# Kernel tuning notes

Hardware: AMD Instinct MI355X
Metric: run time of the kernel (lower is better)

## Reference

```python
import jax, jax.numpy as jnp
import numpy as np

H = 16      # num_heads
DK = 128    # head_dim_qk
DV = 128    # head_dim_v
HID = 2048  # hidden_size
KS = 4      # conv kernel size


def _causal_dwconv(x, w, b):
    # x: [B, T, C], w: [C, KS], b: [C] -- depthwise causal conv (torch pads KS-1 then slices [:T])
    xc = jnp.transpose(x, (0, 2, 1))  # [B, C, T]
    out = jax.lax.conv_general_dilated(
        xc, w[:, None, :], window_strides=(1,), padding=[(KS - 1, 0)],
        feature_group_count=xc.shape[1], dimension_numbers=('NCH', 'OIH', 'NCH'))
    out = out + b[None, :, None]
    return jnp.transpose(out, (0, 2, 1))


def setup_inputs() -> dict:
    key = jax.random.key(0)
    ks = jax.random.split(key, 16)
    s = 0.02
    inp = {
        'x':   jax.random.normal(ks[0], (4, 2048, HID), jnp.float32),
        'Wq':  jax.random.normal(ks[1], (HID, H * DK), jnp.float32) * s,
        'Wk':  jax.random.normal(ks[2], (HID, H * DK), jnp.float32) * s,
        'Wv':  jax.random.normal(ks[3], (HID, H * DV), jnp.float32) * s,
        'Wa':  jax.random.normal(ks[4], (HID, H), jnp.float32) * s,
        'ba':  jnp.zeros((H,), jnp.float32),
        'Wb':  jax.random.normal(ks[5], (HID, H), jnp.float32) * s,
        'bb':  jnp.zeros((H,), jnp.float32),
        'Wg':  jax.random.normal(ks[6], (HID, H * DV), jnp.float32) * s,
        'Wo':  jax.random.normal(ks[7], (H * DV, HID), jnp.float32) * s,
        'qcw': jax.random.normal(ks[8], (H * DK, KS), jnp.float32) * 0.3,
        'qcb': jnp.zeros((H * DK,), jnp.float32),
        'kcw': jax.random.normal(ks[9], (H * DK, KS), jnp.float32) * 0.3,
        'kcb': jnp.zeros((H * DK,), jnp.float32),
        'vcw': jax.random.normal(ks[10], (H * DV, KS), jnp.float32) * 0.3,
        'vcb': jnp.zeros((H * DV,), jnp.float32),
        'ln_w': jnp.ones((DV,), jnp.float32),
        'ln_b': jnp.zeros((DV,), jnp.float32),
    }
    return inp


def _forward(x, Wq, Wk, Wv, Wa, ba, Wb, bb, Wg, Wo, qcw, qcb, kcw, kcb, vcw, vcb, ln_w, ln_b):
    B, T, _ = x.shape
    q = jax.nn.silu(_causal_dwconv(x @ Wq, qcw, qcb))
    k = jax.nn.silu(_causal_dwconv(x @ Wk, kcw, kcb))
    v = jax.nn.silu(_causal_dwconv(x @ Wv, vcw, vcb))
    q = q.reshape(B, T, H, DK)
    k = k.reshape(B, T, H, DK) * (DK ** -0.5)
    v = v.reshape(B, T, H, DV)
    alpha = jax.nn.sigmoid(x @ Wa + ba)  # [B, T, H]
    beta = jax.nn.sigmoid(x @ Wb + bb)   # [B, T, H]

    # time-major for scan
    qT = jnp.transpose(q, (1, 0, 2, 3))
    kT = jnp.transpose(k, (1, 0, 2, 3))
    vT = jnp.transpose(v, (1, 0, 2, 3))
    aT = jnp.transpose(alpha, (1, 0, 2))
    bT = jnp.transpose(beta, (1, 0, 2))

    def step(S, inps):
        qt, kt, vt, at, bt = inps
        Sk = jnp.einsum('bhvk,bhk->bhv', S, kt)            # S @ k
        err = Sk - vt
        S = at[..., None, None] * S - bt[..., None, None] * (err[..., None] * kt[:, :, None, :])
        ot = jnp.einsum('bhvk,bhk->bhv', S, qt)            # output uses NEW state
        return S, ot

    S0 = jnp.zeros((B, H, DV, DK), x.dtype)
    _, oT = jax.lax.scan(step, S0, (qT, kT, vT, aT, bT))    # [T, B, H, DV]
    o = jnp.transpose(oT, (1, 0, 2, 3))                      # [B, T, H, DV]

    # LayerNorm over head_dim_v (eps=1e-5)
    mu = jnp.mean(o, axis=-1, keepdims=True)
    var = jnp.mean(jnp.square(o - mu), axis=-1, keepdims=True)
    o = (o - mu) * jax.lax.rsqrt(var + 1e-5) * ln_w + ln_b

    g = jax.nn.sigmoid(x @ Wg).reshape(B, T, H, DV)
    o = (o * g).reshape(B, T, H * DV)
    return o @ Wo


def reference(x, Wq, Wk, Wv, Wa, ba, Wb, bb, Wg, Wo, qcw, qcb, kcw, kcb, vcw, vcb, ln_w, ln_b):
    return _forward(x, Wq, Wk, Wv, Wa, ba, Wb, bb, Wg, Wo, qcw, qcb, kcw, kcb, vcw, vcb, ln_w, ln_b)
```

## Files before the change

kernel.cpp:

```cpp
#include <hip/hip_runtime.h>
#include <stdint.h>

#define H_   16
#define DK_  128
#define DV_  128
#define HID_ 2048
#define KS_  4
#define B_   4
#define T_   2048
#define BT_  (B_*T_)
#define QKVC (3*HID_)
#define C_   32
#define RS_  32
#define NC_  (T_/C_)

typedef unsigned short u16;
typedef short  bf16x8 __attribute__((ext_vector_type(8)));
typedef u16    u16x8  __attribute__((ext_vector_type(8)));
typedef u16    u16x4  __attribute__((ext_vector_type(4)));
typedef float  f32x4  __attribute__((ext_vector_type(4)));

__device__ __forceinline__ float b2f(u16 u){
  union { unsigned int i; float f; } v; v.i = ((unsigned int)u) << 16; return v.f;
}
__device__ __forceinline__ u16 f2b(float f){
  unsigned int x = __float_as_uint(f);
  unsigned int r = (x + 0x7FFFu + ((x >> 16) & 1u)) >> 16;
  return (u16)r;
}
__device__ __forceinline__ float sigm(float x){ return 1.0f / (1.0f + __expf(-x)); }

#define MFMA16(a,b,c) __builtin_amdgcn_mfma_f32_16x16x32_bf16((a),(b),(c),0,0,0)

__global__ __launch_bounds__(256) void cvt_x_k(const f32x4* __restrict__ src,
                                               u16x4* __restrict__ dst, int n4)
{
  int i0 = blockIdx.x * 256 + threadIdx.x;
  int stride = gridDim.x * 256;
  for (int i = i0; i < n4; i += stride) {
    f32x4 v = src[i];
    u16x4 r; r[0] = f2b(v[0]); r[1] = f2b(v[1]); r[2] = f2b(v[2]); r[3] = f2b(v[3]);
    dst[i] = r;
  }
}

__global__ __launch_bounds__(256) void cvt_small_k(
    const float* __restrict__ qcw, const float* __restrict__ kcw, const float* __restrict__ vcw,
    const float* __restrict__ qcb, const float* __restrict__ kcb, const float* __restrict__ vcb,
    const float* __restrict__ ba,  const float* __restrict__ bb,
    const float* __restrict__ lnw, const float* __restrict__ lnb,
    u16* __restrict__ canon)
{
  int i = blockIdx.x * 256 + threadIdx.x;
  if (i >= 31008) return;
  float v;
  if (i < 24576) {
    const float* s = (i < 8192) ? qcw : (i < 16384) ? kcw : vcw;
    v = s[i & 8191];
  } else if (i < 30720) {
    int j = i - 24576;
    const float* s = (j < 2048) ? qcb : (j < 4096) ? kcb : vcb;
    v = s[j & 2047];
  } else if (i < 30752) {
    int j = i - 30720;
    v = (j < 16) ? ba[j] : bb[j - 16];
  } else {
    int j = i - 30752;
    v = (j < 128) ? lnw[j] : lnb[j - 128];
  }
  canon[i] = f2b(v);
}

__global__ __launch_bounds__(256) void transpose_b(const float* __restrict__ s0,
                                                   const float* __restrict__ s1,
                                                   const float* __restrict__ s2,
                                                   u16* __restrict__ dst,
                                                   int R, int C)
{
  int z = blockIdx.z;
  const float* src = (z == 0) ? s0 : (z == 1) ? s1 : s2;
  u16* d = dst + (size_t)z * R * C;
  __shared__ u16 t[32][33];
  int bx = blockIdx.x * 32;
  int by = blockIdx.y * 32;
  int lx = threadIdx.x & 31, ly = threadIdx.x >> 5;
  #pragma unroll
  for (int i = 0; i < 4; ++i) {
    int r = by + ly + i * 8, c = bx + lx;
    if (r < R && c < C) t[ly + i * 8][lx] = f2b(src[(size_t)r * C + c]);
  }
  __syncthreads();
  #pragma unroll
  for (int i = 0; i < 4; ++i) {
    int r = bx + ly + i * 8;
    int c = by + lx;
    if (r < C && c < R) d[(size_t)r * R + c] = t[lx][ly + i * 8];
  }
}

__device__ __forceinline__ void gload_lds16(const void* gp, void* lp){
  __builtin_amdgcn_global_load_lds(
      (const __attribute__((address_space(1))) void*)gp,
      (__attribute__((address_space(3))) void*)lp, 16, 0, 0);
}

#define GBM 256
#define GBN 256
#define GBK 64

__global__ __launch_bounds__(512, 2) void gemm256(const u16* __restrict__ A, int lda,
                                                  const u16* __restrict__ Bt, int ldb,
                                                  void* __restrict__ C, int ldc,
                                                  int K, int out_f32)
{
  __shared__ u16 lsA[2][GBM * GBK];
  __shared__ u16 lsB[2][GBN * GBK];
  int tid = threadIdx.x, wid = tid >> 6, lane = tid & 63;
  int l16 = lane & 15, quad = lane >> 4;
  int wr = wid >> 2, wc = wid & 3;

  int nbx = gridDim.x;
  int nwg = nbx * gridDim.y;
  int flat = blockIdx.y * nbx + blockIdx.x;
  int swzid = ((nwg & 7) == 0) ? ((flat & 7) * (nwg >> 3) + (flat >> 3)) : flat;
  int m0 = (swzid / nbx) * GBM;
  int n0 = (swzid % nbx) * GBN;

  f32x4 acc[8][4] = {};

  auto STAGE = [&](int t, int bi){
    int k0 = t * GBK;
    #pragma unroll
    for (int ld = 0; ld < 4; ++ld) {
      int slot = ld * 512 + tid;
      int row = slot >> 3, cg = slot & 7;
      int lofs = (ld * 512 + wid * 64) * 8;
      gload_lds16(A  + (size_t)(m0 + row) * lda + k0 + cg * 8, &lsA[bi][lofs]);
      gload_lds16(Bt + (size_t)(n0 + row) * ldb + k0 + cg * 8, &lsB[bi][lofs]);
    }
  };

  STAGE(0, 0);
  __syncthreads();

  int NT = K / GBK;
  for (int t = 0; t < NT; ++t) {
    int bi = t & 1;
    if (t + 1 < NT) STAGE(t + 1, bi ^ 1);
    const u16* pA = lsA[bi];
    const u16* pB = lsB[bi];
    #pragma unroll
    for (int ks = 0; ks < 2; ++ks) {
      bf16x8 bfr[4];
      #pragma unroll
      for (int ni = 0; ni < 4; ++ni)
        bfr[ni] = *(const bf16x8*)&pB[(wc * 64 + ni * 16 + l16) * GBK + ks * 32 + quad * 8];
      #pragma unroll
      for (int mi = 0; mi < 8; ++mi) {
        bf16x8 af = *(const bf16x8*)&pA[(wr * 128 + mi * 16 + l16) * GBK + ks * 32 + quad * 8];
        #pragma unroll
        for (int ni = 0; ni < 4; ++ni)
          acc[mi][ni] = MFMA16(af, bfr[ni], acc[mi][ni]);
      }
    }
    __syncthreads();
  }

  #pragma unroll
  for (int mi = 0; mi < 8; ++mi)
    #pragma unroll
    for (int ni = 0; ni < 4; ++ni)
      #pragma unroll
      for (int r = 0; r < 4; ++r) {
        int m = m0 + wr * 128 + mi * 16 + quad * 4 + r;
        int n = n0 + wc * 64 + ni * 16 + l16;
        if (out_f32) ((float*)C)[(size_t)m * ldc + n] = acc[mi][ni][r];
        else         ((u16*)C)[(size_t)m * ldc + n] = f2b(acc[mi][ni][r]);
      }
}

__global__ __launch_bounds__(256) void ab_k(const u16* __restrict__ x,
                                            const u16* __restrict__ WabT,
                                            const u16* __restrict__ ba,
                                            const u16* __restrict__ bb,
                                            float* __restrict__ ab)
{
  int j = threadIdx.x & 31, rl = threadIdx.x >> 5;
  int row = blockIdx.x * 8 + rl;
  const u16x8* xr = (const u16x8*)(x + (size_t)row * HID_);
  const u16x8* wr = (const u16x8*)(WabT + (size_t)j * HID_);
  float acc = 0.f;
  for (int k = 0; k < HID_ / 8; ++k) {
    u16x8 xv = xr[k], wv = wr[k];
    #pragma unroll
    for (int i = 0; i < 8; ++i) acc += b2f(xv[i]) * b2f(wv[i]);
  }
  float bias = (j < 16) ? b2f(ba[j]) : b2f(bb[j - 16]);
  float sg = sigm(acc + bias);
  if (j < 16) ab[(size_t)row * 16 + j] = sg;
  else        ab[(size_t)BT_ * 16 + (size_t)row * 16 + (j - 16)] = sg;
}

__global__ __launch_bounds__(256) void conv_silu_k(const u16* __restrict__ in,
                                                   const u16* __restrict__ cwv,
                                                   const u16* __restrict__ cbv,
                                                   u16* __restrict__ out)
{
  int idx  = blockIdx.x * 256 + threadIdx.x;
  int col8 = idx % (QKVC / 8);
  int t    = idx / (QKVC / 8);
  int col  = col8 * 8;
  int s = col >> 11;

  u16 wl[32];
  #pragma unroll
  for (int i = 0; i < 4; ++i)
    *(u16x8*)(wl + i * 8) = *(const u16x8*)(cwv + (size_t)col * KS_ + i * 8);
  u16x8 bv = *(const u16x8*)(cbv + col);

  float acc[8];
  #pragma unroll
  for (int j = 0; j < 8; ++j) acc[j] = b2f(bv[j]);

  #pragma unroll
  for (int tap = 0; tap < KS_; ++tap) {
    int tt = t - 3 + tap;
    if (tt >= 0) {
      u16x8 xv = *(const u16x8*)(in + (size_t)tt * QKVC + col);
      #pragma unroll
      for (int j = 0; j < 8; ++j) acc[j] = fmaf(b2f(xv[j]), b2f(wl[j * 4 + tap]), acc[j]);
    }
  }
  float scale = (s == 1) ? 0.08838834764831845f : 1.0f;
  u16x8 rv;
  #pragma unroll
  for (int j = 0; j < 8; ++j) {
    float a = acc[j];
    rv[j] = f2b(a * sigm(a) * scale);
  }
  *(u16x8*)(out + (size_t)t * QKVC + col) = rv;
}

__global__ __launch_bounds__(256) void chunk_scan_k(const u16* __restrict__ qkv,
                                                    const float* __restrict__ ab,
                                                    u16* __restrict__ o)
{
  __shared__ __align__(16) char smem[64896];
  u16 (*Kim)[136] = (u16(*)[136])(smem);
  u16 (*Qim)[136] = (u16(*)[136])(smem + 8704);
  u16 (*Sh)[136]  = (u16(*)[136])(smem + 17408);
  u16 (*Sl)[136]  = (u16(*)[136])(smem + 26112);
  u16 (*KT)[40]   = (u16(*)[40])(smem + 34816);
  u16 (*Vim)[32]  = (u16(*)[32])(smem + 45056);
  float (*KK)[36] = (float(*)[36])(smem + 47104);
  float (*KQ)[33] = (float(*)[33])(smem + 51712);
  float (*SK0)[33]= (float(*)[33])(smem + 55936);
  float (*SQ0)[33]= (float(*)[33])(smem + 60160);
  float (*PL4)[4] = (float(*)[4])(smem + 64384);
  float (*U)[33]  = (float(*)[33])(smem + 8704);

  int bid = blockIdx.x;
  int chain = bid & 63, rblk = bid >> 6;
  int b = chain >> 4, h = chain & 15;
  int tid = threadIdx.x, wv = tid >> 6, lane = tid & 63;
  int l16 = lane & 15, quad = lane >> 4;

  const u16* kbase = qkv + (size_t)b * T_ * QKVC + HID_ + h * DK_;
  const u16* qbase = qkv + (size_t)b * T_ * QKVC + h * DK_;
  const u16* vbase = qkv + (size_t)b * T_ * QKVC + 2 * HID_ + h * DV_ + rblk * RS_;
  const float* abase = ab + (size_t)b * T_ * 16 + h;
  const float* bbase = abase + (size_t)BT_ * 16;
  u16* obase = o + (size_t)b * T_ * 2048 + h * DV_ + rblk * RS_;

  f32x4 st[2][2];
  #pragma unroll
  for (int rt = 0; rt < 2; ++rt)
    #pragma unroll
    for (int ct = 0; ct < 2; ++ct)
      #pragma unroll
      for (int r = 0; r < 4; ++r) st[rt][ct][r] = 0.f;

  int jb = tid - 64;
  u16x8 stg[6];
  float avp = 0.f;

  auto LD = [&](int c) {
    int t0 = c * C_;
    if (wv == 0) {
      avp = (lane < 32) ? abase[(size_t)(t0 + lane) * 16]
                        : bbase[(size_t)(t0 + lane - 32) * 16];
    } else {
      #pragma unroll
      for (int it = 0; it < 6; ++it) {
        int j = jb + it * 192;
        if (j < 512) {
          int t = j >> 4, g = j & 15;
          stg[it] = *(const u16x8*)(kbase + (size_t)(t0 + t) * QKVC + g * 8);
        } else if (j < 1024) {
          int j2 = j - 512, t = j2 >> 4, g = j2 & 15;
          stg[it] = *(const u16x8*)(qbase + (size_t)(t0 + t) * QKVC + g * 8);
        } else {
          int j2 = j - 1024, t = j2 >> 2, rg = j2 & 3;
          stg[it] = *(const u16x8*)(vbase + (size_t)(t0 + t) * QKVC + rg * 8);
        }
      }
    }
  };

  LD(0);

  for (int c = 0; c < NC_; ++c) {
    int t0 = c * C_;

    #pragma unroll
    for (int rt = 0; rt < 2; ++rt)
      #pragma unroll
      for (int ct = 0; ct < 2; ++ct)
        #pragma unroll
        for (int r = 0; r < 4; ++r) {
          float s = st[rt][ct][r];
          u16 hi = f2b(s);
          float lo = s - b2f(hi);
          int row = rt * 16 + quad * 4 + r;
          int col = wv * 32 + ct * 16 + l16;
          Sh[row][col] = hi;
          Sl[row][col] = f2b(lo);
        }

    if (wv == 0) {
      float av = avp;
      float p = av;
      #pragma unroll
      for (int d = 1; d < 32; d <<= 1) {
        float up = __shfl_up(p, d);
        if (lane >= d && lane < 32) p *= up;
      }
      float pm1 = __shfl_up(p, 1);
      float bt = __shfl(av, lane + 32);
      if (lane < 32) {
        if (lane == 0) pm1 = 1.f;
        f32x4 g;
        g[0] = bt * pm1; g[1] = bt; g[2] = 1.0f / p; g[3] = p;
        *(f32x4*)PL4[lane] = g;
      }
    } else {
      #pragma unroll
      for (int it = 0; it < 6; ++it) {
        int j = jb + it * 192;
        if (j < 512) {
          int t = j >> 4, g = j & 15;
          *(u16x8*)&Kim[t][g * 8] = stg[it];
          int blk = ((t >> 3) ^ (g & 3)) << 3;
          int tl = t & 7;
          #pragma unroll
          for (int e = 0; e < 8; ++e)
            KT[g * 8 + e][blk + tl] = stg[it][e];
        } else if (j < 1024) {
          int j2 = j - 512, t = j2 >> 4, g = j2 & 15;
          *(u16x8*)&Qim[t][g * 8] = stg[it];
        } else {
          int j2 = j - 1024, t = j2 >> 2, rg = j2 & 3;
          *(u16x8*)&Vim[t][rg * 8] = stg[it];
        }
      }
    }
    if (c + 1 < NC_) LD(c + 1);
    __syncthreads();

    {
      auto dotKK = [&](int mt, int nt) {
        f32x4 acc = {0.f,0.f,0.f,0.f};
        #pragma unroll
        for (int ks = 0; ks < 4; ++ks) {
          bf16x8 A = *(const bf16x8*)&Kim[mt * 16 + l16][ks * 32 + quad * 8];
          bf16x8 B = *(const bf16x8*)&Kim[nt * 16 + l16][ks * 32 + quad * 8];
          acc = MFMA16(A, B, acc);
        }
        #pragma unroll
        for (int r = 0; r < 4; ++r) KK[mt * 16 + quad * 4 + r][nt * 16 + l16] = acc[r];
      };
      auto dotKQ = [&](int mt, int nt) {
        f32x4 acc = {0.f,0.f,0.f,0.f};
        #pragma unroll
        for (int ks = 0; ks < 4; ++ks) {
          bf16x8 A = *(const bf16x8*)&Qim[mt * 16 + l16][ks * 32 + quad * 8];
          bf16x8 B = *(const bf16x8*)&Kim[nt * 16 + l16][ks * 32 + quad * 8];
          acc = MFMA16(A, B, acc);
        }
        #pragma unroll
        for (int r = 0; r < 4; ++r) KQ[mt * 16 + quad * 4 + r][nt * 16 + l16] = acc[r];
      };
      auto dotS = [&](const u16 (*Aarr)[136], int tt, int rr, float (*OUT)[33]) {
        f32x4 acc = {0.f,0.f,0.f,0.f};
        #pragma unroll
        for (int ks = 0; ks < 4; ++ks) {
          bf16x8 A  = *(const bf16x8*)&Aarr[tt * 16 + l16][ks * 32 + quad * 8];
          bf16x8 Bh = *(const bf16x8*)&Sh[rr * 16 + l16][ks * 32 + quad * 8];
          bf16x8 Bl = *(const bf16x8*)&Sl[rr * 16 + l16][ks * 32 + quad * 8];
          acc = MFMA16(A, Bh, acc);
          acc = MFMA16(A, Bl, acc);
        }
        #pragma unroll
        for (int r = 0; r < 4; ++r) OUT[tt * 16 + quad * 4 + r][rr * 16 + l16] = acc[r];
      };
      if (wv == 0)      { dotS(Kim, 0, 0, SK0); dotS(Kim, 1, 0, SK0); dotKK(0, 0); dotKK(1, 0); }
      else if (wv == 1) { dotS(Kim, 0, 1, SK0); dotS(Kim, 1, 1, SK0); dotKK(1, 1); dotKQ(0, 0); }
      else if (wv == 2) { dotS(Qim, 0, 0, SQ0); dotS(Qim, 1, 0, SQ0); dotKQ(1, 0); }
      else              { dotS(Qim, 0, 1, SQ0); dotS(Qim, 1, 1, SQ0); dotKQ(1, 1); }
    }
    __syncthreads();

    union { u16x8 u; bf16x8 b; } gh, gl;
    if (wv == 0) {
      if (lane < 32) {
        float ub[C_];
        #pragma unroll
        for (int t = 0; t < C_; ++t) {
          f32x4 g = *(const f32x4*)PL4[t];
          float u = g[0] * SK0[t][lane] - g[1] * b2f(Vim[t][lane]);
          float acc = 0.f;
          #pragma unroll
          for (int i4 = 0; i4 < t / 4; ++i4) {
            f32x4 kk = *(const f32x4*)&KK[t][i4 * 4];
            acc = fmaf(kk[0], ub[i4 * 4 + 0], acc);
            acc = fmaf(kk[1], ub[i4 * 4 + 1], acc);
            acc = fmaf(kk[2], ub[i4 * 4 + 2], acc);
            acc = fmaf(kk[3], ub[i4 * 4 + 3], acc);
          }
          #pragma unroll
          for (int i = (t / 4) * 4; i < t; ++i)
            acc = fmaf(KK[t][i], ub[i], acc);
          u = fmaf(-g[0], acc, u);
          U[t][lane] = u;
          ub[t] = g[2] * u;
        }
      }
    } else {
      int mt = wv >> 1, nt = wv & 1; (void)nt;
      int trow = mt * 16 + l16;
      float Pt = PL4[trow][3];
      #pragma unroll
      for (int e = 0; e < 8; ++e) {
        int i = quad * 8 + e;
        float gv = (i <= trow) ? (-Pt * PL4[i][2] * KQ[trow][i]) : 0.f;
        u16 h2 = f2b(gv);
        gh.u[e] = h2; gl.u[e] = f2b(gv - b2f(h2));
      }
    }
    __syncthreads();

    {
      float PL31 = PL4[31][3];

      #pragma unroll
      for (int rt = 0; rt < 2; ++rt) {
        union { u16x8 u; bf16x8 b; } ah, al;
        #pragma unroll
        for (int e = 0; e < 8; ++e) {
          int i = quad * 8 + e;
          float uv = U[i][rt * 16 + l16];
          float ucv = -PL31 * PL4[i][2] * uv;
          u16 hh = f2b(ucv);
          ah.u[e] = hh; al.u[e] = f2b(ucv - b2f(hh));
        }
        #pragma unroll
        for (int ct = 0; ct < 2; ++ct) {
          int col = wv * 32 + ct * 16 + l16;
          bf16x8 Bk = *(const bf16x8*)&KT[col][(quad ^ ((col >> 3) & 3)) << 3];
          f32x4 cacc;
          #pragma unroll
          for (int r = 0; r < 4; ++r) cacc[r] = PL31 * st[rt][ct][r];
          cacc = MFMA16(ah.b, Bk, cacc);
          cacc = MFMA16(al.b, Bk, cacc);
          st[rt][ct] = cacc;
        }
      }

      int mt = wv >> 1, nt = wv & 1;
      if (wv == 0) {
        int trow = mt * 16 + l16;
        float Pt = PL4[trow][3];
        #pragma unroll
        for (int e = 0; e < 8; ++e) {
          int i = quad * 8 + e;
          float gv = (i <= trow) ? (-Pt * PL4[i][2] * KQ[trow][i]) : 0.f;
          u16 h2 = f2b(gv);
          gh.u[e] = h2; gl.u[e] = f2b(gv - b2f(h2));
        }
      }
      union { u16x8 u; bf16x8 b; } uth, utl;
      #pragma unroll
      for (int e = 0; e < 8; ++e) {
        int i = quad * 8 + e;
        float uv = U[i][nt * 16 + l16];
        u16 h1 = f2b(uv);
        uth.u[e] = h1; utl.u[e] = f2b(uv - b2f(h1));
      }
      f32x4 oacc;
      #pragma unroll
      for (int r = 0; r < 4; ++r) {
        int t = mt * 16 + quad * 4 + r;
        oacc[r] = PL4[t][3] * SQ0[t][nt * 16 + l16];
      }
      oacc = MFMA16(gh.b, uth.b, oacc);
      oacc = MFMA16(gh.b, utl.b, oacc);
      oacc = MFMA16(gl.b, uth.b, oacc);
      #pragma unroll
      for (int r = 0; r < 4; ++r) {
        int t = mt * 16 + quad * 4 + r;
        obase[(size_t)(t0 + t) * 2048 + nt * 16 + l16] = f2b(oacc[r]);
      }
    }
    __syncthreads();
  }
}

__global__ __launch_bounds__(256) void ln_gate_k(const u16* __restrict__ o_raw,
                                                 const u16* __restrict__ g,
                                                 const u16* __restrict__ lnw,
                                                 const u16* __restrict__ lnb,
                                                 u16* __restrict__ o_ln)
{
  int gid = blockIdx.x * 4 + (threadIdx.x >> 6);
  int lane = threadIdx.x & 63;
  int row = gid >> 4, h = gid & 15;
  size_t ofs = (size_t)row * 2048 + h * 128 + lane * 2;
  unsigned int e2 = *(const unsigned int*)(o_raw + ofs);
  float ex = b2f((u16)(e2 & 0xffff)), ey = b2f((u16)(e2 >> 16));
  float s = ex + ey, ss = ex * ex + ey * ey;
  #pragma unroll
  for (int m = 1; m < 64; m <<= 1) { s += __shfl_xor(s, m); ss += __shfl_xor(ss, m); }
  float mean = s * (1.f / 128.f);
  float var  = ss * (1.f / 128.f) - mean * mean;
  float rstd = rsqrtf(fmaxf(var, 0.f) + 1e-5f);
  float w0 = b2f(lnw[lane * 2]), w1 = b2f(lnw[lane * 2 + 1]);
  float b0 = b2f(lnb[lane * 2]), b1 = b2f(lnb[lane * 2 + 1]);
  unsigned int g2 = *(const unsigned int*)(g + ofs);
  float g0 = sigm(b2f((u16)(g2 & 0xffff))), g1 = sigm(b2f((u16)(g2 >> 16)));
  float r0 = ((ex - mean) * rstd * w0 + b0) * g0;
  float r1 = ((ey - mean) * rstd * w1 + b1) * g1;
  *(unsigned int*)(o_ln + ofs) = (unsigned int)f2b(r0) | ((unsigned int)f2b(r1) << 16);
}

extern "C" void kernel_launch(void* const* d_in, const int* in_sizes, int n_in,
                              void* d_out, int out_size, void* d_ws, size_t ws_size,
                              hipStream_t stream)
{
  const float* x   = (const float*)d_in[0];
  const float* Wq  = (const float*)d_in[1];
  const float* Wk  = (const float*)d_in[2];
  const float* Wv  = (const float*)d_in[3];
  const float* Wa  = (const float*)d_in[4];
  const float* ba  = (const float*)d_in[5];
  const float* Wb  = (const float*)d_in[6];
  const float* bb  = (const float*)d_in[7];
  const float* Wg  = (const float*)d_in[8];
  const float* Wo  = (const float*)d_in[9];
  const float* qcw = (const float*)d_in[10];
  const float* qcb = (const float*)d_in[11];
  const float* kcw = (const float*)d_in[12];
  const float* kcb = (const float*)d_in[13];
  const float* vcw = (const float*)d_in[14];
  const float* vcb = (const float*)d_in[15];
  const float* lnw = (const float*)d_in[16];
  const float* lnb = (const float*)d_in[17];
  (void)in_sizes; (void)n_in; (void)out_size;

  char* ws = (char*)d_ws;
  size_t off = 0;
  auto alloc = [&](size_t bytes) -> void* {
    void* p = ws + off; off += (bytes + 255) & ~(size_t)255; return p;
  };
  u16* WT    = (u16*)alloc((size_t)3 * HID_ * HID_ * 2);
  u16* WabT  = (u16*)alloc((size_t)32 * HID_ * 2);
  u16* xc    = (u16*)alloc((size_t)BT_ * HID_ * 2);
  u16* canon = (u16*)alloc((size_t)31008 * 2);
  u16* post  = (u16*)alloc((size_t)BT_ * QKVC * 2);
  float* abuf = (float*)alloc((size_t)2 * BT_ * 16 * 4);
  size_t base_off = off;

  size_t fused_need = base_off + (((size_t)BT_ * QKVC * 2 + 255) & ~(size_t)255);
  int fused = (fused_need <= ws_size);
  u16* preC;
  if (fused) preC = (u16*)alloc((size_t)BT_ * QKVC * 2);
  else       preC = (u16*)alloc((size_t)BT_ * HID_ * 2 * 2);
  if (off > ws_size) return;

  u16* cw_c  = canon;
  u16* cb_c  = canon + 24576;
  u16* ba_c  = canon + 30720;
  u16* bb_c  = canon + 30736;
  u16* lnw_c = canon + 30752;
  u16* lnb_c = canon + 30880;

  u16* o_raw = preC;
  u16* g_raw = post;
  u16* o_ln  = post + (size_t)BT_ * HID_;
  u16* WTg   = WT;

  dim3 tb(256), tb5(512);

  cvt_x_k<<<dim3(4096), tb, 0, stream>>>((const f32x4*)x, (u16x4*)xc, BT_ * HID_ / 4);
  cvt_small_k<<<dim3(122), tb, 0, stream>>>(qcw, kcw, vcw, qcb, kcb, vcb, ba, bb, lnw, lnb, canon);

  transpose_b<<<dim3(64, 64, 3), tb, 0, stream>>>(Wq, Wk, Wv, WT, HID_, HID_);
  transpose_b<<<dim3(1, 64, 2), tb, 0, stream>>>(Wa, Wb, Wb, WabT, HID_, 16);

  if (fused) {
    gemm256<<<dim3(QKVC / GBN, BT_ / GBM), tb5, 0, stream>>>(xc, HID_, WT, HID_, preC, QKVC, HID_, 0);
    for (int b = 0; b < B_; ++b)
      conv_silu_k<<<dim3(T_ * (QKVC / 8) / 256), tb, 0, stream>>>(
          preC + (size_t)b * T_ * QKVC, cw_c, cb_c, post + (size_t)b * T_ * QKVC);
  } else {
    for (int b = 0; b < B_; ++b) {
      const u16* xb = xc + (size_t)b * T_ * HID_;
      gemm256<<<dim3(QKVC / GBN, T_ / GBM), tb5, 0, stream>>>(xb, HID_, WT, HID_, preC, QKVC, HID_, 0);
      conv_silu_k<<<dim3(T_ * (QKVC / 8) / 256), tb, 0, stream>>>(
          preC, cw_c, cb_c, post + (size_t)b * T_ * QKVC);
    }
  }

  transpose_b<<<dim3(64, 64, 2), tb, 0, stream>>>(Wg, Wo, Wo, WTg, HID_, HID_);

  ab_k<<<dim3(BT_ / 8), tb, 0, stream>>>(xc, WabT, ba_c, bb_c, abuf);

  chunk_scan_k<<<dim3(256), tb, 0, stream>>>(post, abuf, o_raw);

  gemm256<<<dim3(HID_ / GBN, BT_ / GBM), tb5, 0, stream>>>(xc, HID_, WTg, HID_, g_raw, HID_, HID_, 0);

  ln_gate_k<<<dim3(BT_ * H_ / 4), tb, 0, stream>>>(o_raw, g_raw, lnw_c, lnb_c, o_ln);

  gemm256<<<dim3(HID_ / GBN, BT_ / GBM), tb5, 0, stream>>>(o_ln, HID_,
      WT + (size_t)HID_ * HID_, HID_, d_out, HID_, HID_, 1);
}
```

Before: 1.254 ms.

## Split chunk scan work across eight waves instead of four

The chunked delta-rule scan kernel moves from 256 to 512 threads per block. The state columns, the S·K/S·Q dot tiles, the staging loads and the output tiles are now spread over eight waves, and the output MFMA moves to waves 4-7. The aim is to shorten the per-chunk critical path of the 256-block serial scan by adding parallelism inside each block. The cost is more wave synchronization and possible idle waves, while wave 0's serial U solve stays unchanged.

```diff
diff --git a/kernel.cpp b/kernel.cpp
--- a/kernel.cpp
+++ b/kernel.cpp
@@ -241,7 +241,7 @@
   *(u16x8*)(out + (size_t)t * QKVC + col) = rv;
 }
 
-__global__ __launch_bounds__(256) void chunk_scan_k(const u16* __restrict__ qkv,
+__global__ __launch_bounds__(512) void chunk_scan_k(const u16* __restrict__ qkv,
                                                     const float* __restrict__ ab,
                                                     u16* __restrict__ o)
 {
@@ -272,16 +272,14 @@
   const float* bbase = abase + (size_t)BT_ * 16;
   u16* obase = o + (size_t)b * T_ * 2048 + h * DV_ + rblk * RS_;
 
-  f32x4 st[2][2];
+  f32x4 st[2];
   #pragma unroll
   for (int rt = 0; rt < 2; ++rt)
     #pragma unroll
-    for (int ct = 0; ct < 2; ++ct)
-      #pragma unroll
-      for (int r = 0; r < 4; ++r) st[rt][ct][r] = 0.f;
+    for (int r = 0; r < 4; ++r) st[rt][r] = 0.f;
 
   int jb = tid - 64;
-  u16x8 stg[6];
+  u16x8 stg[3];
   float avp = 0.f;
 
   auto LD = [&](int c) {
@@ -291,15 +289,15 @@
                         : bbase[(size_t)(t0 + lane - 32) * 16];
     } else {
       #pragma unroll
-      for (int it = 0; it < 6; ++it) {
-        int j = jb + it * 192;
+      for (int it = 0; it < 3; ++it) {
+        int j = jb + it * 448;
         if (j < 512) {
           int t = j >> 4, g = j & 15;
           stg[it] = *(const u16x8*)(kbase + (size_t)(t0 + t) * QKVC + g * 8);
         } else if (j < 1024) {
           int j2 = j - 512, t = j2 >> 4, g = j2 & 15;
           stg[it] = *(const u16x8*)(qbase + (size_t)(t0 + t) * QKVC + g * 8);
-        } else {
+        } else if (j < 1152) {
           int j2 = j - 1024, t = j2 >> 2, rg = j2 & 3;
           stg[it] = *(const u16x8*)(vbase + (size_t)(t0 + t) * QKVC + rg * 8);
         }
@@ -315,17 +313,15 @@
     #pragma unroll
     for (int rt = 0; rt < 2; ++rt)
       #pragma unroll
-      for (int ct = 0; ct < 2; ++ct)
-        #pragma unroll
-        for (int r = 0; r < 4; ++r) {
-          float s = st[rt][ct][r];
-          u16 hi = f2b(s);
-          float lo = s - b2f(hi);
-          int row = rt * 16 + quad * 4 + r;
-          int col = wv * 32 + ct * 16 + l16;
-          Sh[row][col] = hi;
-          Sl[row][col] = f2b(lo);
-        }
+      for (int r = 0; r < 4; ++r) {
+        float s = st[rt][r];
+        u16 hi = f2b(s);
+        float lo = s - b2f(hi);
+        int row = rt * 16 + quad * 4 + r;
+        int col = wv * 16 + l16;
+        Sh[row][col] = hi;
+        Sl[row][col] = f2b(lo);
+      }
 
     if (wv == 0) {
       float av = avp;
@@ -345,8 +341,8 @@
       }
     } else {
       #pragma unroll
-      for (int it = 0; it < 6; ++it) {
-        int j = jb + it * 192;
+      for (int it = 0; it < 3; ++it) {
+        int j = jb + it * 448;
         if (j < 512) {
           int t = j >> 4, g = j & 15;
           *(u16x8*)&Kim[t][g * 8] = stg[it];
@@ -358,7 +354,7 @@
         } else if (j < 1024) {
           int j2 = j - 512, t = j2 >> 4, g = j2 & 15;
           *(u16x8*)&Qim[t][g * 8] = stg[it];
-        } else {
+        } else if (j < 1152) {
           int j2 = j - 1024, t = j2 >> 2, rg = j2 & 3;
           *(u16x8*)&Vim[t][rg * 8] = stg[it];
         }
@@ -403,14 +399,21 @@
         #pragma unroll
         for (int r = 0; r < 4; ++r) OUT[tt * 16 + quad * 4 + r][rr * 16 + l16] = acc[r];
       };
-      if (wv == 0)      { dotS(Kim, 0, 0, SK0); dotS(Kim, 1, 0, SK0); dotKK(0, 0); dotKK(1, 0); }
-      else if (wv == 1) { dotS(Kim, 0, 1, SK0); dotS(Kim, 1, 1, SK0); dotKK(1, 1); dotKQ(0, 0); }
-      else if (wv == 2) { dotS(Qim, 0, 0, SQ0); dotS(Qim, 1, 0, SQ0); dotKQ(1, 0); }
-      else              { dotS(Qim, 0, 1, SQ0); dotS(Qim, 1, 1, SQ0); dotKQ(1, 1); }
+      switch (wv) {
+        case 0: dotS(Kim, 0, 0, SK0); dotKK(0, 0); break;
+        case 1: dotS(Kim, 0, 1, SK0); dotKK(1, 0); break;
+        case 2: dotS(Kim, 1, 0, SK0); dotKK(1, 1); break;
+        case 3: dotS(Kim, 1, 1, SK0); dotKQ(0, 0); break;
+        case 4: dotS(Qim, 0, 0, SQ0); dotKQ(1, 0); break;
+        case 5: dotS(Qim, 0, 1, SQ0); dotKQ(1, 1); break;
+        case 6: dotS(Qim, 1, 0, SQ0); break;
+        default: dotS(Qim, 1, 1, SQ0); break;
+      }
     }
     __syncthreads();
 
     union { u16x8 u; bf16x8 b; } gh, gl;
+    int omt = (wv - 4) >> 1, ont = (wv - 4) & 1;
     if (wv == 0) {
       if (lane < 32) {
         float ub[C_];
@@ -435,9 +438,8 @@
           ub[t] = g[2] * u;
         }
       }
-    } else {
-      int mt = wv >> 1, nt = wv & 1; (void)nt;
-      int trow = mt * 16 + l16;
+    } else if (wv >= 4) {
+      int trow = omt * 16 + l16;
       float Pt = PL4[trow][3];
       #pragma unroll
       for (int e = 0; e < 8; ++e) {
@@ -463,52 +465,39 @@
           u16 hh = f2b(ucv);
           ah.u[e] = hh; al.u[e] = f2b(ucv - b2f(hh));
         }
-        #pragma unroll
-        for (int ct = 0; ct < 2; ++ct) {
-          int col = wv * 32 + ct * 16 + l16;
-          bf16x8 Bk = *(const bf16x8*)&KT[col][(quad ^ ((col >> 3) & 3)) << 3];
-          f32x4 cacc;
-          #pragma unroll
-          for (int r = 0; r < 4; ++r) cacc[r] = PL31 * st[rt][ct][r];
-          cacc = MFMA16(ah.b, Bk, cacc);
-          cacc = MFMA16(al.b, Bk, cacc);
-          st[rt][ct] = cacc;
-        }
-      }
-
-      int mt = wv >> 1, nt = wv & 1;
-      if (wv == 0) {
-        int trow = mt * 16 + l16;
-        float Pt = PL4[trow][3];
+        int col = wv * 16 + l16;
+        bf16x8 Bk = *(const bf16x8*)&KT[col][(quad ^ ((col >> 3) & 3)) << 3];
+        f32x4 cacc;
+        #pragma unroll
+        for (int r = 0; r < 4; ++r) cacc[r] = PL31 * st[rt][r];
+        cacc = MFMA16(ah.b, Bk, cacc);
+        cacc = MFMA16(al.b, Bk, cacc);
+        st[rt] = cacc;
+      }
+
+      if (wv >= 4) {
+        union { u16x8 u; bf16x8 b; } uth, utl;
         #pragma unroll
         for (int e = 0; e < 8; ++e) {
           int i = quad * 8 + e;
-          float gv = (i <= trow) ? (-Pt * PL4[i][2] * KQ[trow][i]) : 0.f;
-          u16 h2 = f2b(gv);
-          gh.u[e] = h2; gl.u[e] = f2b(gv - b2f(h2));
-        }
-      }
-      union { u16x8 u; bf16x8 b; } uth, utl;
-      #pragma unroll
-      for (int e = 0; e < 8; ++e) {
-        int i = quad * 8 + e;
-        float uv = U[i][nt * 16 + l16];
-        u16 h1 = f2b(uv);
-        uth.u[e] = h1; utl.u[e] = f2b(uv - b2f(h1));
-      }
-      f32x4 oacc;
-      #pragma unroll
-      for (int r = 0; r < 4; ++r) {
-        int t = mt * 16 + quad * 4 + r;
-        oacc[r] = PL4[t][3] * SQ0[t][nt * 16 + l16];
-      }
-      oacc = MFMA16(gh.b, uth.b, oacc);
-      oacc = MFMA16(gh.b, utl.b, oacc);
-      oacc = MFMA16(gl.b, uth.b, oacc);
-      #pragma unroll
-      for (int r = 0; r < 4; ++r) {
-        int t = mt * 16 + quad * 4 + r;
-        obase[(size_t)(t0 + t) * 2048 + nt * 16 + l16] = f2b(oacc[r]);
+          float uv = U[i][ont * 16 + l16];
+          u16 h1 = f2b(uv);
+          uth.u[e] = h1; utl.u[e] = f2b(uv - b2f(h1));
+        }
+        f32x4 oacc;
+        #pragma unroll
+        for (int r = 0; r < 4; ++r) {
+          int t = omt * 16 + quad * 4 + r;
+          oacc[r] = PL4[t][3] * SQ0[t][ont * 16 + l16];
+        }
+        oacc = MFMA16(gh.b, uth.b, oacc);
+        oacc = MFMA16(gh.b, utl.b, oacc);
+        oacc = MFMA16(gl.b, uth.b, oacc);
+        #pragma unroll
+        for (int r = 0; r < 4; ++r) {
+          int t = omt * 16 + quad * 4 + r;
+          obase[(size_t)(t0 + t) * 2048 + ont * 16 + l16] = f2b(oacc[r]);
+        }
       }
     }
     __syncthreads();
@@ -624,7 +613,7 @@
 
   ab_k<<<dim3(BT_ / 8), tb, 0, stream>>>(xc, WabT, ba_c, bb_c, abuf);
 
-  chunk_scan_k<<<dim3(256), tb, 0, stream>>>(post, abuf, o_raw);
+  chunk_scan_k<<<dim3(256), tb5, 0, stream>>>(post, abuf, o_raw);
 
   gemm256<<<dim3(HID_ / GBN, BT_ / GBM), tb5, 0, stream>>>(xc, HID_, WTg, HID_, g_raw, HID_, HID_, 0);
 
```

After: 1.233 ms. About the same (-1.6%).
